# Kernel tuning notes

Measured on AMD Instinct MI355X. Metric: run time of the kernel, lower is better.

The kernel has to match this reference:

```python
import jax, jax.numpy as jnp
import numpy as np
from jax import lax

B, S, D = 4, 4096, 1024
TOP_K = 2048  # int(S * capacity_factor=0.5)


def setup_inputs() -> dict:
    key = jax.random.key(0)
    k1, k2, k3 = jax.random.split(key, 3)
    x = jax.random.normal(k1, (B, S, D), dtype=jnp.float32)
    # nn.Linear weights (fan-in scaled)
    W_block = jax.random.normal(k2, (D, D), dtype=jnp.float32) / np.sqrt(D)
    W_router = jax.random.normal(k3, (1, D), dtype=jnp.float32) / np.sqrt(D)
    return {"x": x, "W_block": W_block, "W_router": W_router, "top_k": TOP_K}


def reference(x, W_block, W_router, top_k):
    # router logits: [B, S]
    logits = jnp.einsum("bsd,od->bso", x, W_router)[..., 0]
    # top-k token selection along sequence (indices only; unsorted in torch,
    # but index order only permutes which rows are gathered/scattered -> same result)
    _, idx = lax.top_k(logits, top_k)  # [B, K]
    # gather selected tokens: [B, K, D]
    sel = jnp.take_along_axis(x, idx[..., None], axis=1)
    # dense transform (Linear, no bias)
    sel = jnp.einsum("bkd,ed->bke", sel, W_block)
    # scatter transformed tokens back into full tensor (indices are unique)
    batch_idx = jnp.arange(x.shape[0])[:, None]  # [B, 1]
    out = x.at[batch_idx, idx].set(sel)
    return out
```

## Files before the change

### kernel.cpp

```cpp
#include <hip/hip_runtime.h>
#include <hip/hip_bf16.h>
#include <stdint.h>

#define B_ 4
#define S_ 4096
#define D_ 1024
#define TOPK_ 2048
#define NSEL_ (S_ - TOPK_)

#define BM 128
#define BN 128
#define BK 64
#define NT (D_ / BK)
#define GEMM_BLOCKS (B_ * (TOPK_ / BM) * (D_ / BN))
#define COPY_BLOCKS (B_ * NSEL_ / 2)

typedef __attribute__((ext_vector_type(8))) short bf16x8;
typedef __attribute__((ext_vector_type(4))) float f32x4;

__device__ __forceinline__ unsigned pack2bf16(float a, float b) {
  unsigned ua = __float_as_uint(a);
  unsigned ub = __float_as_uint(b);
  ua += 0x7fffu + ((ua >> 16) & 1u);
  ub += 0x7fffu + ((ub >> 16) & 1u);
  return (ua >> 16) | (ub & 0xffff0000u);
}

__device__ __forceinline__ unsigned mono_u32(float f) {
  unsigned u = __float_as_uint(f);
  return (u & 0x80000000u) ? ~u : (u | 0x80000000u);
}

__device__ __forceinline__ void gload_lds16(const void* g, void* l) {
  __builtin_amdgcn_global_load_lds(
      (const __attribute__((address_space(1))) void*)g,
      (__attribute__((address_space(3))) void*)l, 16, 0, 0);
}

__global__ __launch_bounds__(256) void k_router_fused(
    const float* __restrict__ x, const float* __restrict__ wr,
    float* __restrict__ logits, unsigned short* __restrict__ xbf,
    const float* __restrict__ wblock, unsigned short* __restrict__ wbf) {
  const int bid = blockIdx.x;
  if (bid >= B_ * S_ / 4) {
    const int i = (bid - B_ * S_ / 4) * 256 + threadIdx.x;
    float4 v = ((const float4*)wblock)[i];
    *(uint2*)(wbf + (size_t)i * 4) =
        make_uint2(pack2bf16(v.x, v.y), pack2bf16(v.z, v.w));
    return;
  }
  const int lane = threadIdx.x & 63;
  const int token = bid * 4 + (threadIdx.x >> 6);
  const float4* xr = (const float4*)(x + (size_t)token * D_);
  const float4* wrow = (const float4*)wr;
  double acc = 0.0;
#pragma unroll
  for (int i = 0; i < 4; ++i) {
    float4 v = xr[i * 64 + lane];
    float4 w = wrow[i * 64 + lane];
    uint2 p = make_uint2(pack2bf16(v.x, v.y), pack2bf16(v.z, v.w));
    *(uint2*)(xbf + (size_t)token * D_ + i * 256 + lane * 4) = p;
    acc += (double)v.x * (double)w.x + (double)v.y * (double)w.y +
           (double)v.z * (double)w.z + (double)v.w * (double)w.w;
  }
#pragma unroll
  for (int off = 32; off; off >>= 1) acc += __shfl_down(acc, off);
  if (lane == 0) logits[token] = (float)acc;
}

__global__ __launch_bounds__(256) void k_router_plain(
    const float* __restrict__ x, const float* __restrict__ wr,
    float* __restrict__ logits) {
  const int lane = threadIdx.x & 63;
  const int token = blockIdx.x * 4 + (threadIdx.x >> 6);
  const float4* xr = (const float4*)(x + (size_t)token * D_);
  const float4* wrow = (const float4*)wr;
  double acc = 0.0;
#pragma unroll
  for (int i = 0; i < 4; ++i) {
    float4 v = xr[i * 64 + lane];
    float4 w = wrow[i * 64 + lane];
    acc += (double)v.x * (double)w.x + (double)v.y * (double)w.y +
           (double)v.z * (double)w.z + (double)v.w * (double)w.w;
  }
#pragma unroll
  for (int off = 32; off; off >>= 1) acc += __shfl_down(acc, off);
  if (lane == 0) logits[token] = (float)acc;
}

__global__ __launch_bounds__(1024) void k_select(
    const float* __restrict__ logits, unsigned* __restrict__ sel,
    unsigned* __restrict__ notsel) {
  __shared__ unsigned hist[256];
  __shared__ unsigned bc_digit, bc_need;
  __shared__ unsigned scanbuf[17];

  const int b = blockIdx.x;
  const int tid = threadIdx.x;
  const int lane = tid & 63;
  const int wave = tid >> 6;

  float4 v = *(const float4*)(logits + b * S_ + tid * 4);
  unsigned k0 = mono_u32(v.x), k1 = mono_u32(v.y),
           k2 = mono_u32(v.z), k3 = mono_u32(v.w);

  unsigned prefix = 0, need = TOPK_;
#pragma unroll
  for (int pass = 0; pass < 4; ++pass) {
    const int shift = 24 - pass * 8;
    const unsigned maskhi = pass ? (0xFFFFFFFFu << (shift + 8)) : 0u;
    if (tid < 256) hist[tid] = 0;
    __syncthreads();
    if ((k0 & maskhi) == prefix) atomicAdd(&hist[(k0 >> shift) & 255], 1u);
    if ((k1 & maskhi) == prefix) atomicAdd(&hist[(k1 >> shift) & 255], 1u);
    if ((k2 & maskhi) == prefix) atomicAdd(&hist[(k2 >> shift) & 255], 1u);
    if ((k3 & maskhi) == prefix) atomicAdd(&hist[(k3 >> shift) & 255], 1u);
    __syncthreads();
    if (wave == 0) {
      uint4 h = *(const uint4*)(hist + lane * 4);
      unsigned t = h.x + h.y + h.z + h.w;
      unsigned inc = t;
#pragma unroll
      for (int off = 1; off < 64; off <<= 1) {
        unsigned u = __shfl_up(inc, off);
        if (lane >= off) inc += u;
      }
      unsigned total = __shfl(inc, 63);
      unsigned above = total - inc;
      unsigned a3 = above;
      unsigned a2 = a3 + h.w;
      unsigned a1 = a2 + h.z;
      unsigned a0 = a1 + h.y;
      if (a3 < need && need <= a3 + h.w) { bc_digit = lane * 4 + 3; bc_need = need - a3; }
      else if (a2 < need && need <= a2 + h.z) { bc_digit = lane * 4 + 2; bc_need = need - a2; }
      else if (a1 < need && need <= a1 + h.y) { bc_digit = lane * 4 + 1; bc_need = need - a1; }
      else if (a0 < need && need <= a0 + h.x) { bc_digit = lane * 4 + 0; bc_need = need - a0; }
    }
    __syncthreads();
    prefix |= bc_digit << shift;
    need = bc_need;
  }

  const unsigned V = prefix;
  const unsigned fneed = need;

  unsigned packed = 0;
  unsigned pk_excl0, pk_excl1, pk_excl2, pk_excl3;
  pk_excl0 = packed; if (k0 > V) packed += 1u << 16; else if (k0 == V) packed += 1u;
  pk_excl1 = packed; if (k1 > V) packed += 1u << 16; else if (k1 == V) packed += 1u;
  pk_excl2 = packed; if (k2 > V) packed += 1u << 16; else if (k2 == V) packed += 1u;
  pk_excl3 = packed; if (k3 > V) packed += 1u << 16; else if (k3 == V) packed += 1u;

  unsigned inc = packed;
#pragma unroll
  for (int off = 1; off < 64; off <<= 1) {
    unsigned u = __shfl_up(inc, off);
    if (lane >= off) inc += u;
  }
  if (lane == 63) scanbuf[wave] = inc;
  __syncthreads();
  if (tid < 16) {
    unsigned t = scanbuf[tid];
    unsigned winc = t;
#pragma unroll
    for (int off = 1; off < 16; off <<= 1) {
      unsigned u = __shfl_up(winc, off);
      if (tid >= off) winc += u;
    }
    scanbuf[tid] = winc - t;
    if (tid == 15) scanbuf[16] = winc;
  }
  __syncthreads();
  const unsigned base = scanbuf[wave] + (inc - packed);
  const unsigned G_total = scanbuf[16] >> 16;

  unsigned* selb = sel + b * TOPK_;
  unsigned* notb = notsel + b * NSEL_;
#pragma unroll
  for (int i = 0; i < 4; ++i) {
    unsigned ki = (i == 0) ? k0 : (i == 1) ? k1 : (i == 2) ? k2 : k3;
    unsigned pe = (i == 0) ? pk_excl0 : (i == 1) ? pk_excl1 : (i == 2) ? pk_excl2 : pk_excl3;
    unsigned s = tid * 4 + i;
    unsigned gtE = (base + pe) >> 16;
    unsigned eqE = (base + pe) & 0xFFFFu;
    if (ki > V) {
      selb[gtE] = s;
    } else if (ki == V && eqE < fneed) {
      selb[G_total + eqE] = s;
    } else {
      unsigned eqTaken = (eqE < fneed) ? eqE : fneed;
      notb[s - gtE - eqTaken] = s;
    }
  }
}

__global__ __launch_bounds__(512) void k_gemm_copy(
    const unsigned short* __restrict__ xbf, const unsigned short* __restrict__ wbf,
    const unsigned* __restrict__ sel, const unsigned* __restrict__ notsel,
    const float* __restrict__ x, float* __restrict__ out) {
  __shared__ __align__(16) unsigned short Alds[2][BM * BK];
  __shared__ __align__(16) unsigned short Blds[2][BN * BK];

  const int bid = blockIdx.x;
  const int tid = threadIdx.x;

  if (bid >= GEMM_BLOCKS) {
    const int r = (bid - GEMM_BLOCKS) * 2 + (tid >> 8);
    const int b = r >> 11;
    const unsigned s = notsel[r];
    const size_t off = ((size_t)b * S_ + s) * D_;
    ((float4*)(out + off))[tid & 255] = ((const float4*)(x + off))[tid & 255];
    return;
  }

  const int gtile = (bid & 7) * 64 + (bid >> 3);
  const int mtile = gtile >> 3;
  const int nb = gtile & 7;
  const int b = mtile >> 4;
  const int mb = mtile & 15;

  const unsigned* selb = sel + b * TOPK_;
  const unsigned short* xb = xbf + (size_t)b * S_ * D_;
  float* outb = out + (size_t)b * S_ * D_;

  const int lane = tid & 63;
  const int wid = tid >> 6;
  const int wm = wid >> 1;
  const int wn = wid & 1;

  const unsigned short* asrc[2];
  const unsigned short* bsrc[2];
  unsigned ldsoff[2];
#pragma unroll
  for (int r = 0; r < 2; ++r) {
    int chunk = r * 512 + tid;
    int row = chunk >> 3, c16 = chunk & 7;
    int sw = c16 ^ (row & 7);
    asrc[r] = xb + (size_t)selb[mb * BM + row] * D_ + sw * 8;
    bsrc[r] = wbf + (size_t)(nb * BN + row) * D_ + sw * 8;
    ldsoff[r] = chunk * 16;
  }

  unsigned aoff[2][2], boff[4][2];
#pragma unroll
  for (int mi = 0; mi < 2; ++mi)
#pragma unroll
    for (int kk = 0; kk < 2; ++kk) {
      int rrow = wm * 32 + mi * 16 + (lane & 15);
      int byte = rrow * 128 + kk * 64 + (lane >> 4) * 16;
      aoff[mi][kk] = byte ^ ((rrow & 7) << 4);
    }
#pragma unroll
  for (int nj = 0; nj < 4; ++nj)
#pragma unroll
    for (int kk = 0; kk < 2; ++kk) {
      int rrow = wn * 64 + nj * 16 + (lane & 15);
      int byte = rrow * 128 + kk * 64 + (lane >> 4) * 16;
      boff[nj][kk] = byte ^ ((rrow & 7) << 4);
    }

  f32x4 acc[2][4];
#pragma unroll
  for (int i = 0; i < 2; ++i)
#pragma unroll
    for (int j = 0; j < 4; ++j) acc[i][j] = (f32x4)0.0f;

#pragma unroll
  for (int r = 0; r < 2; ++r) {
    gload_lds16(asrc[r], (char*)&Alds[0][0] + ldsoff[r]);
    gload_lds16(bsrc[r], (char*)&Blds[0][0] + ldsoff[r]);
  }
  __syncthreads();

  int cur = 0;
  for (int t = 0; t < NT; ++t) {
    if (t + 1 < NT) {
      const int koff = (t + 1) * BK;
#pragma unroll
      for (int r = 0; r < 2; ++r) {
        gload_lds16(asrc[r] + koff, (char*)&Alds[cur ^ 1][0] + ldsoff[r]);
        gload_lds16(bsrc[r] + koff, (char*)&Blds[cur ^ 1][0] + ldsoff[r]);
      }
    }
#pragma unroll
    for (int kk = 0; kk < 2; ++kk) {
      bf16x8 af[2], bfr[4];
#pragma unroll
      for (int mi = 0; mi < 2; ++mi)
        af[mi] = *(const bf16x8*)((const char*)&Alds[cur][0] + aoff[mi][kk]);
#pragma unroll
      for (int nj = 0; nj < 4; ++nj)
        bfr[nj] = *(const bf16x8*)((const char*)&Blds[cur][0] + boff[nj][kk]);
#pragma unroll
      for (int mi = 0; mi < 2; ++mi)
#pragma unroll
        for (int nj = 0; nj < 4; ++nj)
          acc[mi][nj] = __builtin_amdgcn_mfma_f32_16x16x32_bf16(af[mi], bfr[nj], acc[mi][nj], 0, 0, 0);
    }
    __syncthreads();
    cur ^= 1;
  }

#pragma unroll
  for (int mi = 0; mi < 2; ++mi) {
#pragma unroll
    for (int j = 0; j < 4; ++j) {
      int m = mb * BM + wm * 32 + mi * 16 + (lane >> 4) * 4 + j;
      unsigned srow = selb[m];
      float* orow = outb + (size_t)srow * D_;
#pragma unroll
      for (int nj = 0; nj < 4; ++nj) {
        int col = nb * BN + wn * 64 + nj * 16 + (lane & 15);
        orow[col] = acc[mi][nj][j];
      }
    }
  }
}

__global__ __launch_bounds__(256) void k_copy_rows(
    const float* __restrict__ x, const unsigned* __restrict__ notsel,
    float* __restrict__ out) {
  const int r = blockIdx.x;
  const int b = r >> 11;
  const unsigned s = notsel[r];
  const size_t off = ((size_t)b * S_ + s) * D_;
  ((float4*)(out + off))[threadIdx.x] = ((const float4*)(x + off))[threadIdx.x];
}

__global__ __launch_bounds__(512) void k_gemm_reg(
    const float* __restrict__ x, const float* __restrict__ w,
    const unsigned* __restrict__ sel, float* __restrict__ out) {
  __shared__ __align__(16) unsigned short Alds[BM * BK];
  __shared__ __align__(16) unsigned short Blds[BN * BK];

  const int bid = blockIdx.x;
  const int b = bid >> 7;
  const int rem = bid & 127;
  const int mb = rem >> 3;
  const int nb = rem & 7;

  const unsigned* selb = sel + b * TOPK_;
  const float* xb = x + (size_t)b * S_ * D_;
  float* outb = out + (size_t)b * S_ * D_;

  const int tid = threadIdx.x;
  const int lane = tid & 63;
  const int wid = tid >> 6;
  const int wm = wid >> 1;
  const int wn = wid & 1;

  const float* asrc[4];
  const float* bsrc[4];
  int srow_[4], sc4_[4];
#pragma unroll
  for (int r = 0; r < 4; ++r) {
    int flat = r * 512 + tid;
    int row = flat >> 4;
    int c4 = flat & 15;
    srow_[r] = row;
    sc4_[r] = c4;
    asrc[r] = xb + (size_t)selb[mb * BM + row] * D_ + c4 * 4;
    bsrc[r] = w + (size_t)(nb * BN + row) * D_ + c4 * 4;
  }

  f32x4 acc[2][4];
#pragma unroll
  for (int i = 0; i < 2; ++i)
#pragma unroll
    for (int j = 0; j < 4; ++j) acc[i][j] = (f32x4)0.0f;

  float4 pa[4], pb[4];
#pragma unroll
  for (int r = 0; r < 4; ++r) {
    pa[r] = *(const float4*)(asrc[r]);
    pb[r] = *(const float4*)(bsrc[r]);
  }

  for (int t = 0; t < NT; ++t) {
#pragma unroll
    for (int r = 0; r < 4; ++r) {
      int row = srow_[r], c4 = sc4_[r];
      int byte = row * 128 + c4 * 8;
      byte ^= (row & 7) << 4;
      *(uint2*)((char*)Alds + byte) = make_uint2(pack2bf16(pa[r].x, pa[r].y), pack2bf16(pa[r].z, pa[r].w));
      *(uint2*)((char*)Blds + byte) = make_uint2(pack2bf16(pb[r].x, pb[r].y), pack2bf16(pb[r].z, pb[r].w));
    }
    __syncthreads();

    if (t + 1 < NT) {
      const int koff = (t + 1) * BK;
#pragma unroll
      for (int r = 0; r < 4; ++r) {
        pa[r] = *(const float4*)(asrc[r] + koff);
        pb[r] = *(const float4*)(bsrc[r] + koff);
      }
    }

#pragma unroll
    for (int kk = 0; kk < 2; ++kk) {
      bf16x8 af[2], bfr[4];
#pragma unroll
      for (int mi = 0; mi < 2; ++mi) {
        int rrow = wm * 32 + mi * 16 + (lane & 15);
        int byte = rrow * 128 + (kk * 32 + (lane >> 4) * 8) * 2;
        byte ^= (rrow & 7) << 4;
        af[mi] = *(const bf16x8*)((const char*)Alds + byte);
      }
#pragma unroll
      for (int nj = 0; nj < 4; ++nj) {
        int rrow = wn * 64 + nj * 16 + (lane & 15);
        int byte = rrow * 128 + (kk * 32 + (lane >> 4) * 8) * 2;
        byte ^= (rrow & 7) << 4;
        bfr[nj] = *(const bf16x8*)((const char*)Blds + byte);
      }
#pragma unroll
      for (int mi = 0; mi < 2; ++mi)
#pragma unroll
        for (int nj = 0; nj < 4; ++nj)
          acc[mi][nj] = __builtin_amdgcn_mfma_f32_16x16x32_bf16(af[mi], bfr[nj], acc[mi][nj], 0, 0, 0);
    }
    __syncthreads();
  }

#pragma unroll
  for (int mi = 0; mi < 2; ++mi) {
#pragma unroll
    for (int j = 0; j < 4; ++j) {
      int m = mb * BM + wm * 32 + mi * 16 + (lane >> 4) * 4 + j;
      unsigned srow = selb[m];
      float* orow = outb + (size_t)srow * D_;
#pragma unroll
      for (int nj = 0; nj < 4; ++nj) {
        int col = nb * BN + wn * 64 + nj * 16 + (lane & 15);
        orow[col] = acc[mi][nj][j];
      }
    }
  }
}

extern "C" void kernel_launch(void* const* d_in, const int* in_sizes, int n_in,
                              void* d_out, int out_size, void* d_ws, size_t ws_size,
                              hipStream_t stream) {
  (void)in_sizes; (void)n_in; (void)out_size;
  const float* x = (const float*)d_in[0];
  const float* wb = (const float*)d_in[1];
  const float* wr = (const float*)d_in[2];
  float* out = (float*)d_out;

  char* ws = (char*)d_ws;
  float* logits = (float*)ws;
  unsigned* sel = (unsigned*)(ws + 65536);
  unsigned* notsel = sel + (size_t)B_ * TOPK_;
  unsigned short* xbf = (unsigned short*)(ws + 131072);
  unsigned short* wbf = (unsigned short*)(ws + 131072 + (size_t)B_ * S_ * D_ * 2);
  const size_t NEED = 131072 + (size_t)B_ * S_ * D_ * 2 + (size_t)D_ * D_ * 2;
  const bool fast = ws_size >= NEED;

  if (fast) {
    k_router_fused<<<B_ * S_ / 4 + D_ * D_ / 1024, 256, 0, stream>>>(x, wr, logits, xbf, wb, wbf);
    k_select<<<B_, 1024, 0, stream>>>(logits, sel, notsel);
    k_gemm_copy<<<GEMM_BLOCKS + COPY_BLOCKS, 512, 0, stream>>>(xbf, wbf, sel, notsel, x, out);
  } else {
    k_router_plain<<<B_ * S_ / 4, 256, 0, stream>>>(x, wr, logits);
    k_select<<<B_, 1024, 0, stream>>>(logits, sel, notsel);
    k_copy_rows<<<B_ * NSEL_, 256, 0, stream>>>(x, notsel, out);
    k_gemm_reg<<<GEMM_BLOCKS, 512, 0, stream>>>(x, wb, sel, out);
  }
}
```

Before: 58.37 us.

## Enlarge GEMM tile to 256x128 with triple-buffered LDS prefetch pipeline

The fused GEMM+copy kernel now uses a 256x128 output tile (4x4 MFMA fragments per wave) and a three-stage LDS ring, issuing global-to-LDS loads two k-steps ahead. Full __syncthreads are replaced with explicit vmcnt waits plus raw barriers. The block-index swizzle is updated for the halved number of GEMM blocks. The aim is more reuse of each B tile and better hiding of load latency. The cost is higher LDS use (96KB) and more accumulator registers, which may reduce occupancy, and fewer GEMM blocks (256) for the GPU's CUs.

```diff
diff --git a/kernel.cpp b/kernel.cpp
--- a/kernel.cpp
+++ b/kernel.cpp
@@ -8,12 +8,17 @@
 #define TOPK_ 2048
 #define NSEL_ (S_ - TOPK_)
 
+#define BK 64
+#define NT (D_ / BK)
+
+#define BM2 256
+#define BN2 128
+#define GEMM2_BLOCKS (B_ * (TOPK_ / BM2) * (D_ / BN2))
+#define COPY2_BLOCKS (B_ * NSEL_ / 2)
+
 #define BM 128
 #define BN 128
-#define BK 64
-#define NT (D_ / BK)
-#define GEMM_BLOCKS (B_ * (TOPK_ / BM) * (D_ / BN))
-#define COPY_BLOCKS (B_ * NSEL_ / 2)
+#define GEMM_BLOCKS_FB (B_ * (TOPK_ / BM) * (D_ / BN))
 
 typedef __attribute__((ext_vector_type(8))) short bf16x8;
 typedef __attribute__((ext_vector_type(4))) float f32x4;
@@ -194,18 +199,18 @@
   }
 }
 
-__global__ __launch_bounds__(512) void k_gemm_copy(
+__global__ __launch_bounds__(512, 2) void k_gemm_copy2(
     const unsigned short* __restrict__ xbf, const unsigned short* __restrict__ wbf,
     const unsigned* __restrict__ sel, const unsigned* __restrict__ notsel,
     const float* __restrict__ x, float* __restrict__ out) {
-  __shared__ __align__(16) unsigned short Alds[2][BM * BK];
-  __shared__ __align__(16) unsigned short Blds[2][BN * BK];
+  __shared__ __align__(16) unsigned short Al[3][BM2 * BK];
+  __shared__ __align__(16) unsigned short Bl[3][BN2 * BK];
 
   const int bid = blockIdx.x;
   const int tid = threadIdx.x;
 
-  if (bid >= GEMM_BLOCKS) {
-    const int r = (bid - GEMM_BLOCKS) * 2 + (tid >> 8);
+  if (bid >= GEMM2_BLOCKS) {
+    const int r = (bid - GEMM2_BLOCKS) * 2 + (tid >> 8);
     const int b = r >> 11;
     const unsigned s = notsel[r];
     const size_t off = ((size_t)b * S_ + s) * D_;
@@ -213,11 +218,10 @@
     return;
   }
 
-  const int gtile = (bid & 7) * 64 + (bid >> 3);
-  const int mtile = gtile >> 3;
-  const int nb = gtile & 7;
-  const int b = mtile >> 4;
-  const int mb = mtile & 15;
+  const int swz = (bid & 7) * (GEMM2_BLOCKS / 8) + (bid >> 3);
+  const int b = swz >> 6;
+  const int mt = (swz >> 3) & 7;
+  const int nt = swz & 7;
 
   const unsigned* selb = sel + b * TOPK_;
   const unsigned short* xb = xbf + (size_t)b * S_ * D_;
@@ -228,25 +232,32 @@
   const int wm = wid >> 1;
   const int wn = wid & 1;
 
-  const unsigned short* asrc[2];
+  const unsigned short* asrc[4];
   const unsigned short* bsrc[2];
-  unsigned ldsoff[2];
+  unsigned ldsA[4], ldsB[2];
+#pragma unroll
+  for (int r = 0; r < 4; ++r) {
+    int chunk = r * 512 + tid;
+    int row = chunk >> 3, c16 = chunk & 7;
+    int sw = c16 ^ (row & 7);
+    asrc[r] = xb + (size_t)selb[mt * BM2 + row] * D_ + sw * 8;
+    ldsA[r] = chunk * 16;
+  }
 #pragma unroll
   for (int r = 0; r < 2; ++r) {
     int chunk = r * 512 + tid;
     int row = chunk >> 3, c16 = chunk & 7;
     int sw = c16 ^ (row & 7);
-    asrc[r] = xb + (size_t)selb[mb * BM + row] * D_ + sw * 8;
-    bsrc[r] = wbf + (size_t)(nb * BN + row) * D_ + sw * 8;
-    ldsoff[r] = chunk * 16;
-  }
-
-  unsigned aoff[2][2], boff[4][2];
-#pragma unroll
-  for (int mi = 0; mi < 2; ++mi)
+    bsrc[r] = wbf + (size_t)(nt * BN2 + row) * D_ + sw * 8;
+    ldsB[r] = chunk * 16;
+  }
+
+  unsigned aoff[4][2], boff[4][2];
+#pragma unroll
+  for (int mi = 0; mi < 4; ++mi)
 #pragma unroll
     for (int kk = 0; kk < 2; ++kk) {
-      int rrow = wm * 32 + mi * 16 + (lane & 15);
+      int rrow = wm * 64 + mi * 16 + (lane & 15);
       int byte = rrow * 128 + kk * 64 + (lane >> 4) * 16;
       aoff[mi][kk] = byte ^ ((rrow & 7) << 4);
     }
@@ -259,58 +270,70 @@
       boff[nj][kk] = byte ^ ((rrow & 7) << 4);
     }
 
-  f32x4 acc[2][4];
-#pragma unroll
-  for (int i = 0; i < 2; ++i)
+  f32x4 acc[4][4];
+#pragma unroll
+  for (int i = 0; i < 4; ++i)
 #pragma unroll
     for (int j = 0; j < 4; ++j) acc[i][j] = (f32x4)0.0f;
 
 #pragma unroll
-  for (int r = 0; r < 2; ++r) {
-    gload_lds16(asrc[r], (char*)&Alds[0][0] + ldsoff[r]);
-    gload_lds16(bsrc[r], (char*)&Blds[0][0] + ldsoff[r]);
-  }
-  __syncthreads();
-
-  int cur = 0;
+  for (int r = 0; r < 4; ++r) gload_lds16(asrc[r], (char*)&Al[0][0] + ldsA[r]);
+#pragma unroll
+  for (int r = 0; r < 2; ++r) gload_lds16(bsrc[r], (char*)&Bl[0][0] + ldsB[r]);
+#pragma unroll
+  for (int r = 0; r < 4; ++r) gload_lds16(asrc[r] + BK, (char*)&Al[1][0] + ldsA[r]);
+#pragma unroll
+  for (int r = 0; r < 2; ++r) gload_lds16(bsrc[r] + BK, (char*)&Bl[1][0] + ldsB[r]);
+  asm volatile("s_waitcnt vmcnt(6)" ::: "memory");
+  __builtin_amdgcn_s_barrier();
+  __builtin_amdgcn_sched_barrier(0);
+
+  int c0 = 0, c1 = 1, c2 = 2;
+#pragma unroll 1
   for (int t = 0; t < NT; ++t) {
-    if (t + 1 < NT) {
-      const int koff = (t + 1) * BK;
-#pragma unroll
-      for (int r = 0; r < 2; ++r) {
-        gload_lds16(asrc[r] + koff, (char*)&Alds[cur ^ 1][0] + ldsoff[r]);
-        gload_lds16(bsrc[r] + koff, (char*)&Blds[cur ^ 1][0] + ldsoff[r]);
-      }
-    }
+    if (t + 2 < NT) {
+      const int koff = (t + 2) * BK;
+#pragma unroll
+      for (int r = 0; r < 4; ++r) gload_lds16(asrc[r] + koff, (char*)&Al[c2][0] + ldsA[r]);
+#pragma unroll
+      for (int r = 0; r < 2; ++r) gload_lds16(bsrc[r] + koff, (char*)&Bl[c2][0] + ldsB[r]);
+    }
+    const char* Ab = (const char*)&Al[c0][0];
+    const char* Bb = (const char*)&Bl[c0][0];
 #pragma unroll
     for (int kk = 0; kk < 2; ++kk) {
-      bf16x8 af[2], bfr[4];
-#pragma unroll
-      for (int mi = 0; mi < 2; ++mi)
-        af[mi] = *(const bf16x8*)((const char*)&Alds[cur][0] + aoff[mi][kk]);
-#pragma unroll
-      for (int nj = 0; nj < 4; ++nj)
-        bfr[nj] = *(const bf16x8*)((const char*)&Blds[cur][0] + boff[nj][kk]);
-#pragma unroll
-      for (int mi = 0; mi < 2; ++mi)
+      bf16x8 af[4], bfr[4];
+#pragma unroll
+      for (int mi = 0; mi < 4; ++mi) af[mi] = *(const bf16x8*)(Ab + aoff[mi][kk]);
+#pragma unroll
+      for (int nj = 0; nj < 4; ++nj) bfr[nj] = *(const bf16x8*)(Bb + boff[nj][kk]);
+#pragma unroll
+      for (int mi = 0; mi < 4; ++mi)
 #pragma unroll
         for (int nj = 0; nj < 4; ++nj)
           acc[mi][nj] = __builtin_amdgcn_mfma_f32_16x16x32_bf16(af[mi], bfr[nj], acc[mi][nj], 0, 0, 0);
     }
-    __syncthreads();
-    cur ^= 1;
-  }
-
-#pragma unroll
-  for (int mi = 0; mi < 2; ++mi) {
+    __builtin_amdgcn_sched_barrier(0);
+    if (t + 2 < NT) {
+      asm volatile("s_waitcnt vmcnt(6)" ::: "memory");
+    } else {
+      asm volatile("s_waitcnt vmcnt(0)" ::: "memory");
+    }
+    __builtin_amdgcn_s_barrier();
+    __builtin_amdgcn_sched_barrier(0);
+    int tmp = c0; c0 = c1; c1 = c2; c2 = tmp;
+  }
+
+#pragma unroll
+  for (int mi = 0; mi < 4; ++mi) {
 #pragma unroll
     for (int j = 0; j < 4; ++j) {
-      int m = mb * BM + wm * 32 + mi * 16 + (lane >> 4) * 4 + j;
+      int m = mt * BM2 + wm * 64 + mi * 16 + (lane >> 4) * 4 + j;
       unsigned srow = selb[m];
       float* orow = outb + (size_t)srow * D_;
 #pragma unroll
       for (int nj = 0; nj < 4; ++nj) {
-        int col = nb * BN + wn * 64 + nj * 16 + (lane & 15);
+        int col = nt * BN2 + wn * 64 + nj * 16 + (lane & 15);
         orow[col] = acc[mi][nj][j];
       }
     }
@@ -459,11 +482,11 @@
   if (fast) {
     k_router_fused<<<B_ * S_ / 4 + D_ * D_ / 1024, 256, 0, stream>>>(x, wr, logits, xbf, wb, wbf);
     k_select<<<B_, 1024, 0, stream>>>(logits, sel, notsel);
-    k_gemm_copy<<<GEMM_BLOCKS + COPY_BLOCKS, 512, 0, stream>>>(xbf, wbf, sel, notsel, x, out);
+    k_gemm_copy2<<<GEMM2_BLOCKS + COPY2_BLOCKS, 512, 0, stream>>>(xbf, wbf, sel, notsel, x, out);
   } else {
     k_router_plain<<<B_ * S_ / 4, 256, 0, stream>>>(x, wr, logits);
     k_select<<<B_, 1024, 0, stream>>>(logits, sel, notsel);
     k_copy_rows<<<B_ * NSEL_, 256, 0, stream>>>(x, notsel, out);
-    k_gemm_reg<<<GEMM_BLOCKS, 512, 0, stream>>>(x, wb, sel, out);
-  }
-}
+    k_gemm_reg<<<GEMM_BLOCKS_FB, 512, 0, stream>>>(x, wb, sel, out);
+  }
+}
```

Measured after the change: 67.69 us. 1.16x slower.

## Convert only selected rows to bf16 in a separate prep kernel before GEMM

Applied to the files above, without the earlier changes.

The router no longer converts all of x to bf16. A new prep kernel runs after selection and gathers only the selected rows into a compact contiguous bf16 buffer. The same kernel also copies the unselected rows and converts the weight matrix. The GEMM then reads contiguous A rows without indirection and gets a launch_bounds occupancy hint. This halves the bf16 write traffic, but it adds a kernel launch and re-reads the selected rows of x after the router pass, and the copy no longer overlaps with the GEMM.

```diff
diff --git a/kernel.cpp b/kernel.cpp
--- a/kernel.cpp
+++ b/kernel.cpp
@@ -13,7 +13,10 @@
 #define BK 64
 #define NT (D_ / BK)
 #define GEMM_BLOCKS (B_ * (TOPK_ / BM) * (D_ / BN))
-#define COPY_BLOCKS (B_ * NSEL_ / 2)
+
+#define PREP_CONV (B_ * TOPK_)
+#define PREP_COPY (B_ * NSEL_)
+#define PREP_W    (D_ * D_ / 1024)
 
 typedef __attribute__((ext_vector_type(8))) short bf16x8;
 typedef __attribute__((ext_vector_type(4))) float f32x4;
@@ -37,38 +40,7 @@
       (__attribute__((address_space(3))) void*)l, 16, 0, 0);
 }
 
-__global__ __launch_bounds__(256) void k_router_fused(
-    const float* __restrict__ x, const float* __restrict__ wr,
-    float* __restrict__ logits, unsigned short* __restrict__ xbf,
-    const float* __restrict__ wblock, unsigned short* __restrict__ wbf) {
-  const int bid = blockIdx.x;
-  if (bid >= B_ * S_ / 4) {
-    const int i = (bid - B_ * S_ / 4) * 256 + threadIdx.x;
-    float4 v = ((const float4*)wblock)[i];
-    *(uint2*)(wbf + (size_t)i * 4) =
-        make_uint2(pack2bf16(v.x, v.y), pack2bf16(v.z, v.w));
-    return;
-  }
-  const int lane = threadIdx.x & 63;
-  const int token = bid * 4 + (threadIdx.x >> 6);
-  const float4* xr = (const float4*)(x + (size_t)token * D_);
-  const float4* wrow = (const float4*)wr;
-  double acc = 0.0;
-#pragma unroll
-  for (int i = 0; i < 4; ++i) {
-    float4 v = xr[i * 64 + lane];
-    float4 w = wrow[i * 64 + lane];
-    uint2 p = make_uint2(pack2bf16(v.x, v.y), pack2bf16(v.z, v.w));
-    *(uint2*)(xbf + (size_t)token * D_ + i * 256 + lane * 4) = p;
-    acc += (double)v.x * (double)w.x + (double)v.y * (double)w.y +
-           (double)v.z * (double)w.z + (double)v.w * (double)w.w;
-  }
-#pragma unroll
-  for (int off = 32; off; off >>= 1) acc += __shfl_down(acc, off);
-  if (lane == 0) logits[token] = (float)acc;
-}
-
-__global__ __launch_bounds__(256) void k_router_plain(
+__global__ __launch_bounds__(256) void k_router_logits(
     const float* __restrict__ x, const float* __restrict__ wr,
     float* __restrict__ logits) {
   const int lane = threadIdx.x & 63;
@@ -194,24 +166,45 @@
   }
 }
 
-__global__ __launch_bounds__(512) void k_gemm_copy(
-    const unsigned short* __restrict__ xbf, const unsigned short* __restrict__ wbf,
-    const unsigned* __restrict__ sel, const unsigned* __restrict__ notsel,
-    const float* __restrict__ x, float* __restrict__ out) {
-  __shared__ __align__(16) unsigned short Alds[2][BM * BK];
-  __shared__ __align__(16) unsigned short Blds[2][BN * BK];
-
+__global__ __launch_bounds__(256) void k_prep(
+    const float* __restrict__ x, const unsigned* __restrict__ sel,
+    const unsigned* __restrict__ notsel, const float* __restrict__ wblock,
+    unsigned short* __restrict__ xbfc, unsigned short* __restrict__ wbf,
+    float* __restrict__ out) {
   const int bid = blockIdx.x;
   const int tid = threadIdx.x;
 
-  if (bid >= GEMM_BLOCKS) {
-    const int r = (bid - GEMM_BLOCKS) * 2 + (tid >> 8);
+  if (bid < PREP_CONV) {
+    const int b = bid >> 11;
+    const unsigned srow = sel[bid];
+    const float4* src = (const float4*)(x + ((size_t)b * S_ + srow) * D_);
+    float4 v = src[tid];
+    *(uint2*)(xbfc + (size_t)bid * D_ + tid * 4) =
+        make_uint2(pack2bf16(v.x, v.y), pack2bf16(v.z, v.w));
+    return;
+  }
+  if (bid < PREP_CONV + PREP_COPY) {
+    const int r = bid - PREP_CONV;
     const int b = r >> 11;
     const unsigned s = notsel[r];
     const size_t off = ((size_t)b * S_ + s) * D_;
-    ((float4*)(out + off))[tid & 255] = ((const float4*)(x + off))[tid & 255];
+    ((float4*)(out + off))[tid] = ((const float4*)(x + off))[tid];
     return;
   }
+  const int i = (bid - PREP_CONV - PREP_COPY) * 256 + tid;
+  float4 v = ((const float4*)wblock)[i];
+  *(uint2*)(wbf + (size_t)i * 4) =
+      make_uint2(pack2bf16(v.x, v.y), pack2bf16(v.z, v.w));
+}
+
+__global__ __launch_bounds__(512, 2) void k_gemm(
+    const unsigned short* __restrict__ xbfc, const unsigned short* __restrict__ wbf,
+    const unsigned* __restrict__ sel, float* __restrict__ out) {
+  __shared__ __align__(16) unsigned short Alds[2][BM * BK];
+  __shared__ __align__(16) unsigned short Blds[2][BN * BK];
+
+  const int bid = blockIdx.x;
+  const int tid = threadIdx.x;
 
   const int gtile = (bid & 7) * 64 + (bid >> 3);
   const int mtile = gtile >> 3;
@@ -220,7 +213,7 @@
   const int mb = mtile & 15;
 
   const unsigned* selb = sel + b * TOPK_;
-  const unsigned short* xb = xbf + (size_t)b * S_ * D_;
+  const unsigned short* arows = xbfc + ((size_t)b * TOPK_ + mb * BM) * D_;
   float* outb = out + (size_t)b * S_ * D_;
 
   const int lane = tid & 63;
@@ -236,7 +229,7 @@
     int chunk = r * 512 + tid;
     int row = chunk >> 3, c16 = chunk & 7;
     int sw = c16 ^ (row & 7);
-    asrc[r] = xb + (size_t)selb[mb * BM + row] * D_ + sw * 8;
+    asrc[r] = arows + (size_t)row * D_ + sw * 8;
     bsrc[r] = wbf + (size_t)(nb * BN + row) * D_ + sw * 8;
     ldsoff[r] = chunk * 16;
   }
@@ -451,17 +444,18 @@
   float* logits = (float*)ws;
   unsigned* sel = (unsigned*)(ws + 65536);
   unsigned* notsel = sel + (size_t)B_ * TOPK_;
-  unsigned short* xbf = (unsigned short*)(ws + 131072);
-  unsigned short* wbf = (unsigned short*)(ws + 131072 + (size_t)B_ * S_ * D_ * 2);
-  const size_t NEED = 131072 + (size_t)B_ * S_ * D_ * 2 + (size_t)D_ * D_ * 2;
+  unsigned short* xbfc = (unsigned short*)(ws + 131072);
+  unsigned short* wbf = (unsigned short*)(ws + 131072 + (size_t)B_ * TOPK_ * D_ * 2);
+  const size_t NEED = 131072 + (size_t)B_ * TOPK_ * D_ * 2 + (size_t)D_ * D_ * 2;
   const bool fast = ws_size >= NEED;
 
   if (fast) {
-    k_router_fused<<<B_ * S_ / 4 + D_ * D_ / 1024, 256, 0, stream>>>(x, wr, logits, xbf, wb, wbf);
+    k_router_logits<<<B_ * S_ / 4, 256, 0, stream>>>(x, wr, logits);
     k_select<<<B_, 1024, 0, stream>>>(logits, sel, notsel);
-    k_gemm_copy<<<GEMM_BLOCKS + COPY_BLOCKS, 512, 0, stream>>>(xbf, wbf, sel, notsel, x, out);
+    k_prep<<<PREP_CONV + PREP_COPY + PREP_W, 256, 0, stream>>>(x, sel, notsel, wb, xbfc, wbf, out);
+    k_gemm<<<GEMM_BLOCKS, 512, 0, stream>>>(xbfc, wbf, sel, out);
   } else {
-    k_router_plain<<<B_ * S_ / 4, 256, 0, stream>>>(x, wr, logits);
+    k_router_logits<<<B_ * S_ / 4, 256, 0, stream>>>(x, wr, logits);
     k_select<<<B_, 1024, 0, stream>>>(logits, sel, notsel);
     k_copy_rows<<<B_ * NSEL_, 256, 0, stream>>>(x, notsel, out);
     k_gemm_reg<<<GEMM_BLOCKS, 512, 0, stream>>>(x, wb, sel, out);
```

Measured after the change: 62.59 us. 1.07x slower.
